# Optimization experiments

Hardware: AMD Instinct MI355X
Metric: run time of the kernel (lower is better)

The kernel has to match this reference:

```python
import jax, jax.numpy as jnp
from jax import lax
import numpy as np

WIN = 8          # window side -> N = 64 tokens per window
DIM = 256
HEADS = 8
B_ = 4096        # batch * num_windows
DN = ('NCHW', 'OIHW', 'NCHW')


def _rel_pos_index(win):
    ch = np.arange(win)
    coords = np.stack(np.meshgrid(ch, ch, indexing='ij'))
    flat = coords.reshape(2, -1)
    rel = flat[:, :, None] - flat[:, None, :]                      # [2,N,N]
    rel = rel.transpose(1, 2, 0).astype(np.int32)                  # [N,N,2]
    rel[..., 0] += win - 1
    rel[..., 1] += win - 1
    rel[..., 0] *= 2 * win - 1
    return rel.sum(-1)                                             # [N,N] in [0, (2w-1)^2)


def _sepconv(x, dw_w, dw_b, pw_w, pw_b):
    # x: [B,C,H,W]; depthwise 3x3 (groups=C) + bias + ReLU, then pointwise 1x1 + bias
    C = x.shape[1]
    y = lax.conv_general_dilated(x, dw_w, (1, 1), [(1, 1), (1, 1)],
                                 dimension_numbers=DN, feature_group_count=C)
    y = jax.nn.relu(y + dw_b[None, :, None, None])
    y = lax.conv_general_dilated(y, pw_w, (1, 1), [(0, 0), (0, 0)],
                                 dimension_numbers=DN)
    return y + pw_b[None, :, None, None]


def setup_inputs() -> dict:
    key = jax.random.key(0)
    ks = jax.random.split(key, 16)
    C = DIM
    d = {}
    d['x'] = jax.random.normal(ks[0], (B_, WIN * WIN, C), dtype=jnp.float32)
    for i, p in enumerate(['q', 'k', 'v']):
        d[f'{p}_dw_w'] = jax.random.normal(ks[1 + 4 * i], (C, 1, 3, 3), jnp.float32) * 0.05
        d[f'{p}_dw_b'] = jax.random.normal(ks[2 + 4 * i], (C,), jnp.float32) * 0.02
        d[f'{p}_pw_w'] = jax.random.normal(ks[3 + 4 * i], (C, C, 1, 1), jnp.float32) * 0.05
        d[f'{p}_pw_b'] = jax.random.normal(ks[4 + 4 * i], (C,), jnp.float32) * 0.02
    d['bias_table'] = jax.random.normal(ks[13], ((2 * WIN - 1) ** 2, HEADS), jnp.float32) * 0.02
    d['proj_w'] = jax.random.normal(ks[14], (C, C), jnp.float32) * 0.02
    d['proj_b'] = jax.random.normal(ks[15], (C,), jnp.float32) * 0.02
    d['rel_index'] = jnp.asarray(_rel_pos_index(WIN))  # [N,N] int32
    return d


def reference(x, q_dw_w, q_dw_b, q_pw_w, q_pw_b,
              k_dw_w, k_dw_b, k_pw_w, k_pw_b,
              v_dw_w, v_dw_b, v_pw_w, v_pw_b,
              bias_table, proj_w, proj_b, rel_index):
    B, N, C = x.shape
    H = HEADS
    dh = C // H
    scale = dh ** (-0.5)
    l = WIN
    xi = x.transpose(0, 2, 1).reshape(B, C, l, l)          # b (l w) c -> b c l w
    q = _sepconv(xi, q_dw_w, q_dw_b, q_pw_w, q_pw_b)
    k = _sepconv(xi, k_dw_w, k_dw_b, k_pw_w, k_pw_b)
    v = _sepconv(xi, v_dw_w, v_dw_b, v_pw_w, v_pw_b)
    # b (h d) l w -> b h (l w) d
    q = q.reshape(B, H, dh, N).transpose(0, 1, 3, 2)
    k = k.reshape(B, H, dh, N).transpose(0, 1, 3, 2)
    v = v.reshape(B, H, dh, N).transpose(0, 1, 3, 2)
    attn = jnp.einsum('bhnd,bhmd->bhnm', q * scale, k)     # [B,H,N,N]
    bias = bias_table[rel_index]                           # [N,N,H] gather
    attn = attn + bias.transpose(2, 0, 1)[None]            # ratio=1, repeat is identity
    attn = jax.nn.softmax(attn, axis=-1)
    out = jnp.einsum('bhnm,bhmd->bhnd', attn, v)           # [B,H,N,dh]
    out = out.transpose(0, 2, 1, 3).reshape(B, N, C)
    return out @ proj_w.T + proj_b
```

## Files before the change

### kernel.cpp

```cpp
#include <hip/hip_runtime.h>

typedef __attribute__((ext_vector_type(8))) short bf16x8;
typedef __attribute__((ext_vector_type(4))) float f32x4;

#define XK_B 0
#define S_B  32768
#define Q_B  49152

__device__ __forceinline__ unsigned short f2b(float f) {
  unsigned int v = __builtin_bit_cast(unsigned int, f);
  v += 0x7FFFu + ((v >> 16) & 1u);
  return (unsigned short)(v >> 16);
}
__device__ __forceinline__ unsigned int pk2(float a, float b) {
  return (unsigned int)f2b(a) | ((unsigned int)f2b(b) << 16);
}
__device__ __forceinline__ bf16x8 pack8(const float4& a, const float4& b) {
  union { unsigned int u[4]; bf16x8 v; } x;
  x.u[0] = pk2(a.x, a.y); x.u[1] = pk2(a.z, a.w);
  x.u[2] = pk2(b.x, b.y); x.u[3] = pk2(b.z, b.w);
  return x.v;
}
__device__ __forceinline__ float lo16(unsigned int u) { return __builtin_bit_cast(float, u << 16); }
__device__ __forceinline__ float hi16(unsigned int u) { return __builtin_bit_cast(float, u & 0xFFFF0000u); }

__global__ void transpose_dw_kernel(const float* __restrict__ w0,
                                    const float* __restrict__ w1,
                                    const float* __restrict__ w2,
                                    float* __restrict__ out) {
  int i = blockIdx.x * 256 + threadIdx.x;
  if (i >= 6912) return;
  int p = i / 2304, r = i % 2304, tap = r >> 8, c = r & 255;
  const float* w = (p == 0) ? w0 : ((p == 1) ? w1 : w2);
  out[i] = w[c * 9 + tap];
}

template<int USE_WS>
__global__ __launch_bounds__(512, 2) void winattn_kernel(
    const float* __restrict__ xg,
    const float* __restrict__ dww0, const float* __restrict__ dwb0,
    const float* __restrict__ pww0, const float* __restrict__ pwb0,
    const float* __restrict__ dww1, const float* __restrict__ dwb1,
    const float* __restrict__ pww1, const float* __restrict__ pwb1,
    const float* __restrict__ dww2, const float* __restrict__ dwb2,
    const float* __restrict__ pww2, const float* __restrict__ pwb2,
    const float* __restrict__ bt,
    const float* __restrict__ pjw, const float* __restrict__ pjb,
    const int* __restrict__ rel,
    const float* __restrict__ wsT,
    float* __restrict__ outg)
{
  __shared__ __align__(16) unsigned char smem[81920];

  const int tid  = threadIdx.x;
  const int lane = tid & 63;
  const int wv   = tid >> 6;
  const int lc   = lane & 15;
  const int lq2  = lane >> 4;
  const int b    = blockIdx.x;
  const float* xb = xg + (size_t)b * 16384;

  const f32x4 zero4 = {0.f, 0.f, 0.f, 0.f};

#pragma unroll
  for (int it = 0; it < 4; ++it) {
    const int g   = tid + it * 512;
    const int n   = g >> 5;
    const int c16 = g & 31;
    const float4 wa = *(const float4*)(xb + n * 256 + c16 * 8);
    const float4 wb = *(const float4*)(xb + n * 256 + c16 * 8 + 4);
    *(bf16x8*)(smem + XK_B + n * 512 + ((c16 ^ (n & 7))) * 16) = pack8(wa, wb);
  }
  __syncthreads();

  auto dwconv = [&](int s, const float* __restrict__ dwb,
                    const float* __restrict__ dwwT, const float* __restrict__ dwwR) {
    const int c4    = tid & 31;
    const int strip = tid >> 5;
    const int l   = strip >> 1;
    const int w0c = (strip & 1) * 4;
    const int cb  = s * 128 + c4 * 4;
    const int c16 = s * 16 + (c4 >> 1);
    const int hb8 = (c4 & 1) * 8;
    float o[4][4];
    {
      const f32x4 bv = *(const f32x4*)(dwb + cb);
#pragma unroll
      for (int t = 0; t < 4; ++t)
#pragma unroll
        for (int j = 0; j < 4; ++j) o[t][j] = bv[j];
    }
#pragma unroll
    for (int dl = 0; dl < 3; ++dl) {
      const int row = l + dl - 1;
      const bool rok = (row >= 0) && (row < 8);
      float wt[3][4];
#pragma unroll
      for (int dc = 0; dc < 3; ++dc) {
        if (USE_WS) {
          const f32x4 wv0 = *(const f32x4*)(dwwT + (dl * 3 + dc) * 256 + cb);
#pragma unroll
          for (int j = 0; j < 4; ++j) wt[dc][j] = wv0[j];
        } else {
#pragma unroll
          for (int j = 0; j < 4; ++j) wt[dc][j] = dwwR[(cb + j) * 9 + dl * 3 + dc];
        }
      }
#pragma unroll
      for (int jc = 0; jc < 6; ++jc) {
        const int col = w0c + jc - 1;
        float xc[4];
        if (rok && col >= 0 && col < 8) {
          const int t = row * 8 + col;
          const uint2 u = *(const uint2*)(smem + XK_B + t * 512 + ((c16 ^ (t & 7))) * 16 + hb8);
          xc[0] = lo16(u.x); xc[1] = hi16(u.x);
          xc[2] = lo16(u.y); xc[3] = hi16(u.y);
        } else {
#pragma unroll
          for (int j = 0; j < 4; ++j) xc[j] = 0.f;
        }
#pragma unroll
        for (int dc = 0; dc < 3; ++dc) {
          const int ot = jc - dc;
          if (ot >= 0 && ot < 4) {
#pragma unroll
            for (int j = 0; j < 4; ++j) o[ot][j] = fmaf(wt[dc][j], xc[j], o[ot][j]);
          }
        }
      }
    }
#pragma unroll
    for (int t = 0; t < 4; ++t) {
      const int n = l * 8 + w0c + t;
      uint2 u;
      u.x = pk2(fmaxf(o[t][0], 0.f), fmaxf(o[t][1], 0.f));
      u.y = pk2(fmaxf(o[t][2], 0.f), fmaxf(o[t][3], 0.f));
      *(uint2*)(smem + S_B + n * 256 + (((c4 >> 1) ^ (n & 15)) & 15) * 16 + hb8) = u;
    }
  };

  bf16x8 vfrag[2][2];
  {
    f32x4 av[4][2];
#pragma unroll
    for (int i = 0; i < 4; ++i)
#pragma unroll
      for (int t = 0; t < 2; ++t) av[i][t] = zero4;

#pragma unroll 1
    for (int s = 0; s < 2; ++s) {
      dwconv(s, dwb2, USE_WS ? (wsT + 2 * 2304) : nullptr, dww2);
      __syncthreads();
      const float* W = pww2;
#pragma unroll
      for (int kk = 0; kk < 4; ++kk) {
        bf16x8 afr[4];
#pragma unroll
        for (int i = 0; i < 4; ++i) {
          const int m = 16 * i + lc;
          afr[i] = *(const bf16x8*)(smem + S_B + m * 256 + (((4 * kk + lq2) ^ (m & 15)) & 15) * 16);
        }
        bf16x8 bb[2];
#pragma unroll
        for (int t = 0; t < 2; ++t) {
          const int co = 16 * (2 * wv + t) + lc;
          const int ci0 = s * 128 + 32 * kk + 8 * lq2;
          const float4 wa = *(const float4*)(W + co * 256 + ci0);
          const float4 wb = *(const float4*)(W + co * 256 + ci0 + 4);
          bb[t] = pack8(wa, wb);
        }
#pragma unroll
        for (int i = 0; i < 4; ++i)
#pragma unroll
          for (int t = 0; t < 2; ++t)
            av[i][t] = __builtin_amdgcn_mfma_f32_16x16x32_bf16(afr[i], bb[t], av[i][t], 0, 0, 0);
      }
      __syncthreads();
    }
#pragma unroll
    for (int t = 0; t < 2; ++t) {
      const float pb = pwb2[16 * (2 * wv + t) + lc];
#pragma unroll
      for (int i = 0; i < 4; ++i) {
        const int m0 = 16 * i + 4 * lq2;
        uint2 u;
        u.x = pk2(av[i][t][0] + pb, av[i][t][1] + pb);
        u.y = pk2(av[i][t][2] + pb, av[i][t][3] + pb);
        *(uint2*)(smem + S_B + wv * 2048 + lc * 128 +
                  (((m0 >> 3) ^ (lc & 7)) & 7) * 16 + (lq2 & 1) * 8) = u;
      }
#pragma unroll
      for (int kk = 0; kk < 2; ++kk)
        vfrag[t][kk] = *(const bf16x8*)(smem + S_B + wv * 2048 + lc * 128 +
                                        (((4 * kk + lq2) ^ (lc & 7)) & 7) * 16);
    }
  }
  __syncthreads();

#pragma unroll 1
  for (int qk = 0; qk < 2; ++qk) {
    const int dstB = qk ? XK_B : Q_B;
    const float* W   = qk ? pww1 : pww0;
    const float* pwb = qk ? pwb1 : pwb0;
    const float* dwb = qk ? dwb1 : dwb0;
    const float* dwT = USE_WS ? (wsT + qk * 2304) : nullptr;
    const float* dwR = qk ? dww1 : dww0;
    f32x4 acc[2][4];
#pragma unroll
    for (int cot = 0; cot < 2; ++cot)
#pragma unroll
      for (int nt = 0; nt < 4; ++nt) acc[cot][nt] = zero4;

#pragma unroll 1
    for (int s = 0; s < 2; ++s) {
      dwconv(s, dwb, dwT, dwR);
      __syncthreads();
#pragma unroll
      for (int kk = 0; kk < 4; ++kk) {
        bf16x8 afrW[2];
#pragma unroll
        for (int cot = 0; cot < 2; ++cot) {
          const int co = 32 * wv + 16 * cot + lc;
          const int ci0 = s * 128 + 32 * kk + 8 * lq2;
          const float4 wa = *(const float4*)(W + co * 256 + ci0);
          const float4 wb = *(const float4*)(W + co * 256 + ci0 + 4);
          afrW[cot] = pack8(wa, wb);
        }
        bf16x8 bfr[4];
#pragma unroll
        for (int nt = 0; nt < 4; ++nt) {
          const int n = 16 * nt + lc;
          bfr[nt] = *(const bf16x8*)(smem + S_B + n * 256 + (((4 * kk + lq2) ^ (n & 15)) & 15) * 16);
        }
#pragma unroll
        for (int cot = 0; cot < 2; ++cot)
#pragma unroll
          for (int nt = 0; nt < 4; ++nt)
            acc[cot][nt] = __builtin_amdgcn_mfma_f32_16x16x32_bf16(afrW[cot], bfr[nt], acc[cot][nt], 0, 0, 0);
      }
      __syncthreads();
    }
#pragma unroll
    for (int cot = 0; cot < 2; ++cot) {
      const int c0 = 32 * wv + 16 * cot + 4 * lq2;
      const f32x4 pb = *(const f32x4*)(pwb + c0);
#pragma unroll
      for (int nt = 0; nt < 4; ++nt) {
        const int n = 16 * nt + lc;
        uint2 u;
        u.x = pk2(acc[cot][nt][0] + pb[0], acc[cot][nt][1] + pb[1]);
        u.y = pk2(acc[cot][nt][2] + pb[2], acc[cot][nt][3] + pb[3]);
        *(uint2*)(smem + dstB + n * 512 + (((c0 >> 3) ^ (n & 31)) & 31) * 16 + (lq2 & 1) * 8) = u;
      }
    }
  }

  {
    const int h = wv;
    bf16x8 kfrag[4];
#pragma unroll
    for (int mt = 0; mt < 4; ++mt) {
      const int m = 16 * mt + lc;
      kfrag[mt] = *(const bf16x8*)(smem + XK_B + m * 512 + (((4 * h + lq2) ^ (m & 31)) & 31) * 16);
    }
    const float scale = 0.17677669529663687f;
#pragma unroll
    for (int qt = 0; qt < 4; ++qt) {
      const int n = 16 * qt + lc;
      const bf16x8 qfrag = *(const bf16x8*)(smem + Q_B + n * 512 + (((4 * h + lq2) ^ (n & 31)) & 31) * 16);
      f32x4 sc[4];
#pragma unroll
      for (int mt = 0; mt < 4; ++mt)
        sc[mt] = __builtin_amdgcn_mfma_f32_16x16x32_bf16(kfrag[mt], qfrag, zero4, 0, 0, 0);
      const int* relrow = rel + n * 64;
      float sv[4][4];
#pragma unroll
      for (int mt = 0; mt < 4; ++mt)
#pragma unroll
        for (int r = 0; r < 4; ++r) {
          const int m = 16 * mt + 4 * lq2 + r;
          sv[mt][r] = sc[mt][r] * scale + bt[relrow[m] * 8 + h];
        }
      float mx = sv[0][0];
#pragma unroll
      for (int mt = 0; mt < 4; ++mt)
#pragma unroll
        for (int r = 0; r < 4; ++r) mx = fmaxf(mx, sv[mt][r]);
      mx = fmaxf(mx, __shfl_xor(mx, 16));
      mx = fmaxf(mx, __shfl_xor(mx, 32));
      float sum = 0.f;
#pragma unroll
      for (int mt = 0; mt < 4; ++mt)
#pragma unroll
        for (int r = 0; r < 4; ++r) {
          sv[mt][r] = __expf(sv[mt][r] - mx);
          sum += sv[mt][r];
        }
      sum += __shfl_xor(sum, 16);
      sum += __shfl_xor(sum, 32);
      const float rinv = __builtin_amdgcn_rcpf(sum);
#pragma unroll
      for (int mt = 0; mt < 4; ++mt) {
        const int m0 = 16 * mt + 4 * lq2;
        uint2 u;
        u.x = pk2(sv[mt][0], sv[mt][1]);
        u.y = pk2(sv[mt][2], sv[mt][3]);
        *(uint2*)(smem + S_B + wv * 2048 + lc * 128 +
                  (((m0 >> 3) ^ (lc & 7)) & 7) * 16 + (lq2 & 1) * 8) = u;
      }
      f32x4 o[2] = {zero4, zero4};
#pragma unroll
      for (int kk = 0; kk < 2; ++kk) {
        const bf16x8 pf = *(const bf16x8*)(smem + S_B + wv * 2048 + lc * 128 +
                                           (((4 * kk + lq2) ^ (lc & 7)) & 7) * 16);
#pragma unroll
        for (int ct = 0; ct < 2; ++ct)
          o[ct] = __builtin_amdgcn_mfma_f32_16x16x32_bf16(vfrag[ct][kk], pf, o[ct], 0, 0, 0);
      }
#pragma unroll
      for (int ct = 0; ct < 2; ++ct) {
        const int c0 = 32 * h + 16 * ct + 4 * lq2;
        uint2 u;
        u.x = pk2(o[ct][0] * rinv, o[ct][1] * rinv);
        u.y = pk2(o[ct][2] * rinv, o[ct][3] * rinv);
        *(uint2*)(smem + XK_B + n * 512 + (((c0 >> 3) ^ (n & 31)) & 31) * 16 + (lq2 & 1) * 8) = u;
      }
    }
  }
  __syncthreads();

  {
    f32x4 pacc[4][2];
#pragma unroll
    for (int i = 0; i < 4; ++i)
#pragma unroll
      for (int t = 0; t < 2; ++t) pacc[i][t] = zero4;
#pragma unroll
    for (int kk = 0; kk < 8; ++kk) {
      bf16x8 afr[4];
#pragma unroll
      for (int i = 0; i < 4; ++i) {
        const int n = 16 * i + lc;
        afr[i] = *(const bf16x8*)(smem + XK_B + n * 512 + (((4 * kk + lq2) ^ (n & 31)) & 31) * 16);
      }
      bf16x8 bb[2];
#pragma unroll
      for (int t = 0; t < 2; ++t) {
        const int co = 16 * (2 * wv + t) + lc;
        const float4 wa = *(const float4*)(pjw + co * 256 + 32 * kk + 8 * lq2);
        const float4 wb = *(const float4*)(pjw + co * 256 + 32 * kk + 8 * lq2 + 4);
        bb[t] = pack8(wa, wb);
      }
#pragma unroll
      for (int i = 0; i < 4; ++i)
#pragma unroll
        for (int t = 0; t < 2; ++t)
          pacc[i][t] = __builtin_amdgcn_mfma_f32_16x16x32_bf16(afr[i], bb[t], pacc[i][t], 0, 0, 0);
    }
    float* og = outg + (size_t)b * 16384;
#pragma unroll
    for (int t = 0; t < 2; ++t) {
      const int co = 16 * (2 * wv + t) + lc;
      const float pbv = pjb[co];
#pragma unroll
      for (int i = 0; i < 4; ++i)
#pragma unroll
        for (int r = 0; r < 4; ++r)
          og[(16 * i + 4 * lq2 + r) * 256 + co] = pacc[i][t][r] + pbv;
    }
  }
}

extern "C" void kernel_launch(void* const* d_in, const int* in_sizes, int n_in,
                              void* d_out, int out_size, void* d_ws, size_t ws_size,
                              hipStream_t stream) {
  (void)in_sizes; (void)n_in; (void)out_size;
  const float* x    = (const float*)d_in[0];
  const float* qdww = (const float*)d_in[1];
  const float* qdwb = (const float*)d_in[2];
  const float* qpww = (const float*)d_in[3];
  const float* qpwb = (const float*)d_in[4];
  const float* kdww = (const float*)d_in[5];
  const float* kdwb = (const float*)d_in[6];
  const float* kpww = (const float*)d_in[7];
  const float* kpwb = (const float*)d_in[8];
  const float* vdww = (const float*)d_in[9];
  const float* vdwb = (const float*)d_in[10];
  const float* vpww = (const float*)d_in[11];
  const float* vpwb = (const float*)d_in[12];
  const float* bt   = (const float*)d_in[13];
  const float* pjw  = (const float*)d_in[14];
  const float* pjb  = (const float*)d_in[15];
  const int* rel    = (const int*)d_in[16];
  float* out        = (float*)d_out;

  const bool use_ws = (ws_size >= 6912 * sizeof(float)) && (d_ws != nullptr);
  float* wsT = (float*)d_ws;

  if (use_ws) {
    hipLaunchKernelGGL(transpose_dw_kernel, dim3(27), dim3(256), 0, stream,
                       qdww, kdww, vdww, wsT);
    hipLaunchKernelGGL((winattn_kernel<1>), dim3(4096), dim3(512), 0, stream,
                       x, qdww, qdwb, qpww, qpwb, kdww, kdwb, kpww, kpwb,
                       vdww, vdwb, vpww, vpwb, bt, pjw, pjb, rel, wsT, out);
  } else {
    hipLaunchKernelGGL((winattn_kernel<0>), dim3(4096), dim3(512), 0, stream,
                       x, qdww, qdwb, qpww, qpwb, kdww, kdwb, kpww, kpwb,
                       vdww, vdwb, vpww, vpwb, bt, pjw, pjb, rel, (const float*)nullptr, out);
  }
}
```

Measured before the change: 954.8 us.

## Split fused window attention into QKV and attention+projection kernels via workspace

Splits the single fused kernel into two. The first computes the Q/K/V separable convolutions and writes bf16 fragments to a large global workspace (about 400MB). The second reads those fragments, runs attention with the relative-position bias and softmax, then applies the output projection. This is meant to cut shared memory per block (49KB instead of 80KB) so more blocks fit per CU, at the cost of extra global memory traffic. The split path runs only when the harness workspace is large enough; otherwise the fused kernel is used.

```diff
diff --git a/kernel.cpp b/kernel.cpp
--- a/kernel.cpp
+++ b/kernel.cpp
@@ -6,6 +6,10 @@
 #define XK_B 0
 #define S_B  32768
 #define Q_B  49152
+#define K1_S 32768
+#define K2_P 32768
+
+#define QWS_SHORTS 67108864ull
 
 __device__ __forceinline__ unsigned short f2b(float f) {
   unsigned int v = __builtin_bit_cast(unsigned int, f);
@@ -35,6 +39,363 @@
   out[i] = w[c * 9 + tap];
 }
 
+__global__ __launch_bounds__(512, 2) void qkv_kernel(
+    const float* __restrict__ xg,
+    const float* __restrict__ dwb0, const float* __restrict__ pww0, const float* __restrict__ pwb0,
+    const float* __restrict__ dwb1, const float* __restrict__ pww1, const float* __restrict__ pwb1,
+    const float* __restrict__ dwb2, const float* __restrict__ pww2, const float* __restrict__ pwb2,
+    const float* __restrict__ dwT,
+    unsigned short* __restrict__ qkv)
+{
+  __shared__ __align__(16) unsigned char smem[49152];
+  const int tid  = threadIdx.x;
+  const int lane = tid & 63;
+  const int wv   = tid >> 6;
+  const int lc   = lane & 15;
+  const int lq2  = lane >> 4;
+  const int b    = blockIdx.x;
+  const float* xb = xg + (size_t)b * 16384;
+  const f32x4 zero4 = {0.f, 0.f, 0.f, 0.f};
+
+#pragma unroll
+  for (int it = 0; it < 4; ++it) {
+    const int g   = tid + it * 512;
+    const int n   = g >> 5;
+    const int c16 = g & 31;
+    const float4 wa = *(const float4*)(xb + n * 256 + c16 * 8);
+    const float4 wb = *(const float4*)(xb + n * 256 + c16 * 8 + 4);
+    *(bf16x8*)(smem + XK_B + n * 512 + ((c16 ^ (n & 7))) * 16) = pack8(wa, wb);
+  }
+  __syncthreads();
+
+  auto dwconv = [&](int s, const float* __restrict__ dwb, const float* __restrict__ dT) {
+    const int c4    = tid & 31;
+    const int strip = tid >> 5;
+    const int l   = strip >> 1;
+    const int w0c = (strip & 1) * 4;
+    const int cb  = s * 128 + c4 * 4;
+    const int c16 = s * 16 + (c4 >> 1);
+    const int hb8 = (c4 & 1) * 8;
+    float o[4][4];
+    {
+      const f32x4 bv = *(const f32x4*)(dwb + cb);
+#pragma unroll
+      for (int t = 0; t < 4; ++t)
+#pragma unroll
+        for (int j = 0; j < 4; ++j) o[t][j] = bv[j];
+    }
+#pragma unroll
+    for (int dl = 0; dl < 3; ++dl) {
+      const int row = l + dl - 1;
+      const bool rok = (row >= 0) && (row < 8);
+      float wt[3][4];
+#pragma unroll
+      for (int dc = 0; dc < 3; ++dc) {
+        const f32x4 wv0 = *(const f32x4*)(dT + (dl * 3 + dc) * 256 + cb);
+#pragma unroll
+        for (int j = 0; j < 4; ++j) wt[dc][j] = wv0[j];
+      }
+#pragma unroll
+      for (int jc = 0; jc < 6; ++jc) {
+        const int col = w0c + jc - 1;
+        float xc[4];
+        if (rok && col >= 0 && col < 8) {
+          const int t = row * 8 + col;
+          const uint2 u = *(const uint2*)(smem + XK_B + t * 512 + ((c16 ^ (t & 7))) * 16 + hb8);
+          xc[0] = lo16(u.x); xc[1] = hi16(u.x);
+          xc[2] = lo16(u.y); xc[3] = hi16(u.y);
+        } else {
+#pragma unroll
+          for (int j = 0; j < 4; ++j) xc[j] = 0.f;
+        }
+#pragma unroll
+        for (int dc = 0; dc < 3; ++dc) {
+          const int ot = jc - dc;
+          if (ot >= 0 && ot < 4) {
+#pragma unroll
+            for (int j = 0; j < 4; ++j) o[ot][j] = fmaf(wt[dc][j], xc[j], o[ot][j]);
+          }
+        }
+      }
+    }
+#pragma unroll
+    for (int t = 0; t < 4; ++t) {
+      const int n = l * 8 + w0c + t;
+      uint2 u;
+      u.x = pk2(fmaxf(o[t][0], 0.f), fmaxf(o[t][1], 0.f));
+      u.y = pk2(fmaxf(o[t][2], 0.f), fmaxf(o[t][3], 0.f));
+      *(uint2*)(smem + K1_S + n * 256 + (((c4 >> 1) ^ (n & 15)) & 15) * 16 + hb8) = u;
+    }
+  };
+
+#pragma unroll 1
+  for (int qk = 0; qk < 2; ++qk) {
+    const float* W   = qk ? pww1 : pww0;
+    const float* pwb = qk ? pwb1 : pwb0;
+    const float* dwb = qk ? dwb1 : dwb0;
+    const float* dT  = dwT + qk * 2304;
+    f32x4 acc[2][4];
+#pragma unroll
+    for (int cot = 0; cot < 2; ++cot)
+#pragma unroll
+      for (int nt = 0; nt < 4; ++nt) acc[cot][nt] = zero4;
+
+#pragma unroll 1
+    for (int s = 0; s < 2; ++s) {
+      dwconv(s, dwb, dT);
+      __syncthreads();
+#pragma unroll
+      for (int kk = 0; kk < 4; ++kk) {
+        bf16x8 afrW[2];
+#pragma unroll
+        for (int cot = 0; cot < 2; ++cot) {
+          const int co = 32 * wv + 16 * cot + lc;
+          const int ci0 = s * 128 + 32 * kk + 8 * lq2;
+          const float4 wa = *(const float4*)(W + co * 256 + ci0);
+          const float4 wb = *(const float4*)(W + co * 256 + ci0 + 4);
+          afrW[cot] = pack8(wa, wb);
+        }
+        bf16x8 bfr[4];
+#pragma unroll
+        for (int nt = 0; nt < 4; ++nt) {
+          const int n = 16 * nt + lc;
+          bfr[nt] = *(const bf16x8*)(smem + K1_S + n * 256 + (((4 * kk + lq2) ^ (n & 15)) & 15) * 16);
+        }
+#pragma unroll
+        for (int cot = 0; cot < 2; ++cot)
+#pragma unroll
+          for (int nt = 0; nt < 4; ++nt)
+            acc[cot][nt] = __builtin_amdgcn_mfma_f32_16x16x32_bf16(afrW[cot], bfr[nt], acc[cot][nt], 0, 0, 0);
+      }
+      __syncthreads();
+    }
+    unsigned short* dst = qkv + (qk ? QWS_SHORTS : 0) + ((size_t)(b * 8 + wv) * 4) * 512;
+    unsigned char* Sb = smem + K1_S + wv * 2048;
+#pragma unroll
+    for (int rr = 0; rr < 2; ++rr) {
+#pragma unroll
+      for (int cot = 0; cot < 2; ++cot) {
+        const int c0 = 32 * wv + 16 * cot + 4 * lq2;
+        const f32x4 pb = *(const f32x4*)(pwb + c0);
+        const int o8 = 2 * cot + (lq2 >> 1);
+#pragma unroll
+        for (int nt2 = 0; nt2 < 2; ++nt2) {
+          const int nt = 2 * rr + nt2;
+          const int nn = 16 * nt2 + lc;
+          uint2 u;
+          u.x = pk2(acc[cot][nt][0] + pb[0], acc[cot][nt][1] + pb[1]);
+          u.y = pk2(acc[cot][nt][2] + pb[2], acc[cot][nt][3] + pb[3]);
+          *(uint2*)(Sb + nn * 64 + ((o8 ^ (nn & 3)) * 16) + (lq2 & 1) * 8) = u;
+        }
+      }
+#pragma unroll
+      for (int mtl = 0; mtl < 2; ++mtl) {
+        const int nn = 16 * mtl + lc;
+        const bf16x8 fr = *(const bf16x8*)(Sb + nn * 64 + ((lq2 ^ (nn & 3)) * 16));
+        *(bf16x8*)(dst + (2 * rr + mtl) * 512 + lane * 8) = fr;
+      }
+    }
+    __syncthreads();
+  }
+
+  {
+    f32x4 av[4][2];
+#pragma unroll
+    for (int i = 0; i < 4; ++i)
+#pragma unroll
+      for (int t = 0; t < 2; ++t) av[i][t] = zero4;
+
+#pragma unroll 1
+    for (int s = 0; s < 2; ++s) {
+      dwconv(s, dwb2, dwT + 2 * 2304);
+      __syncthreads();
+#pragma unroll
+      for (int kk = 0; kk < 4; ++kk) {
+        bf16x8 afr[4];
+#pragma unroll
+        for (int i = 0; i < 4; ++i) {
+          const int m = 16 * i + lc;
+          afr[i] = *(const bf16x8*)(smem + K1_S + m * 256 + (((4 * kk + lq2) ^ (m & 15)) & 15) * 16);
+        }
+        bf16x8 bb[2];
+#pragma unroll
+        for (int t = 0; t < 2; ++t) {
+          const int co = 16 * (2 * wv + t) + lc;
+          const int ci0 = s * 128 + 32 * kk + 8 * lq2;
+          const float4 wa = *(const float4*)(pww2 + co * 256 + ci0);
+          const float4 wb = *(const float4*)(pww2 + co * 256 + ci0 + 4);
+          bb[t] = pack8(wa, wb);
+        }
+#pragma unroll
+        for (int i = 0; i < 4; ++i)
+#pragma unroll
+          for (int t = 0; t < 2; ++t)
+            av[i][t] = __builtin_amdgcn_mfma_f32_16x16x32_bf16(afr[i], bb[t], av[i][t], 0, 0, 0);
+      }
+      __syncthreads();
+    }
+    unsigned short* dst = qkv + 2 * QWS_SHORTS + ((size_t)(b * 8 + wv) * 4) * 512;
+#pragma unroll
+    for (int t = 0; t < 2; ++t) {
+      const float pb = pwb2[16 * (2 * wv + t) + lc];
+#pragma unroll
+      for (int i = 0; i < 4; ++i) {
+        const int m0 = 16 * i + 4 * lq2;
+        uint2 u;
+        u.x = pk2(av[i][t][0] + pb, av[i][t][1] + pb);
+        u.y = pk2(av[i][t][2] + pb, av[i][t][3] + pb);
+        *(uint2*)(smem + K1_S + wv * 2048 + lc * 128 +
+                  (((m0 >> 3) ^ (lc & 7)) & 7) * 16 + (lq2 & 1) * 8) = u;
+      }
+#pragma unroll
+      for (int kk = 0; kk < 2; ++kk) {
+        const bf16x8 vf = *(const bf16x8*)(smem + K1_S + wv * 2048 + lc * 128 +
+                                           (((4 * kk + lq2) ^ (lc & 7)) & 7) * 16);
+        *(bf16x8*)(dst + (t * 2 + kk) * 512 + lane * 8) = vf;
+      }
+    }
+  }
+}
+
+__global__ __launch_bounds__(512, 2) void attnproj_kernel(
+    const unsigned short* __restrict__ qkv,
+    const float* __restrict__ bt,
+    const float* __restrict__ pjw, const float* __restrict__ pjb,
+    const int* __restrict__ rel,
+    float* __restrict__ outg)
+{
+  __shared__ __align__(16) unsigned char smem[49152];
+  const int tid  = threadIdx.x;
+  const int lane = tid & 63;
+  const int wv   = tid >> 6;
+  const int lc   = lane & 15;
+  const int lq2  = lane >> 4;
+  const int b    = blockIdx.x;
+  const f32x4 zero4 = {0.f, 0.f, 0.f, 0.f};
+
+  const unsigned short* qw = qkv + ((size_t)(b * 8 + wv) * 4) * 512;
+  const unsigned short* kw = qw + QWS_SHORTS;
+  const unsigned short* vw = qw + 2 * QWS_SHORTS;
+
+  bf16x8 kfrag[4];
+#pragma unroll
+  for (int mt = 0; mt < 4; ++mt)
+    kfrag[mt] = *(const bf16x8*)(kw + mt * 512 + lane * 8);
+  bf16x8 vfrag[2][2];
+#pragma unroll
+  for (int t = 0; t < 2; ++t)
+#pragma unroll
+    for (int kk = 0; kk < 2; ++kk)
+      vfrag[t][kk] = *(const bf16x8*)(vw + (t * 2 + kk) * 512 + lane * 8);
+
+  const float scale = 0.17677669529663687f;
+  const int h = wv;
+#pragma unroll
+  for (int qt = 0; qt < 4; ++qt) {
+    const int n = 16 * qt + lc;
+    const bf16x8 qfrag = *(const bf16x8*)(qw + qt * 512 + lane * 8);
+    f32x4 sc[4];
+#pragma unroll
+    for (int mt = 0; mt < 4; ++mt)
+      sc[mt] = __builtin_amdgcn_mfma_f32_16x16x32_bf16(kfrag[mt], qfrag, zero4, 0, 0, 0);
+    const int* relrow = rel + n * 64;
+    float sv[4][4];
+#pragma unroll
+    for (int mt = 0; mt < 4; ++mt)
+#pragma unroll
+      for (int r = 0; r < 4; ++r) {
+        const int m = 16 * mt + 4 * lq2 + r;
+        sv[mt][r] = sc[mt][r] * scale + bt[relrow[m] * 8 + h];
+      }
+    float mx = sv[0][0];
+#pragma unroll
+    for (int mt = 0; mt < 4; ++mt)
+#pragma unroll
+      for (int r = 0; r < 4; ++r) mx = fmaxf(mx, sv[mt][r]);
+    mx = fmaxf(mx, __shfl_xor(mx, 16));
+    mx = fmaxf(mx, __shfl_xor(mx, 32));
+    float sum = 0.f;
+#pragma unroll
+    for (int mt = 0; mt < 4; ++mt)
+#pragma unroll
+      for (int r = 0; r < 4; ++r) {
+        sv[mt][r] = __expf(sv[mt][r] - mx);
+        sum += sv[mt][r];
+      }
+    sum += __shfl_xor(sum, 16);
+    sum += __shfl_xor(sum, 32);
+    const float rinv = __builtin_amdgcn_rcpf(sum);
+#pragma unroll
+    for (int mt = 0; mt < 4; ++mt) {
+      const int m0 = 16 * mt + 4 * lq2;
+      uint2 u;
+      u.x = pk2(sv[mt][0], sv[mt][1]);
+      u.y = pk2(sv[mt][2], sv[mt][3]);
+      *(uint2*)(smem + K2_P + wv * 2048 + lc * 128 +
+                (((m0 >> 3) ^ (lc & 7)) & 7) * 16 + (lq2 & 1) * 8) = u;
+    }
+    f32x4 o[2] = {zero4, zero4};
+#pragma unroll
+    for (int kk = 0; kk < 2; ++kk) {
+      const bf16x8 pf = *(const bf16x8*)(smem + K2_P + wv * 2048 + lc * 128 +
+                                         (((4 * kk + lq2) ^ (lc & 7)) & 7) * 16);
+#pragma unroll
+      for (int ct = 0; ct < 2; ++ct)
+        o[ct] = __builtin_amdgcn_mfma_f32_16x16x32_bf16(vfrag[ct][kk], pf, o[ct], 0, 0, 0);
+    }
+#pragma unroll
+    for (int ct = 0; ct < 2; ++ct) {
+      const int c0 = 32 * h + 16 * ct + 4 * lq2;
+      uint2 u;
+      u.x = pk2(o[ct][0] * rinv, o[ct][1] * rinv);
+      u.y = pk2(o[ct][2] * rinv, o[ct][3] * rinv);
+      *(uint2*)(smem + n * 512 + (((c0 >> 3) ^ (n & 31)) & 31) * 16 + (lq2 & 1) * 8) = u;
+    }
+  }
+  __syncthreads();
+
+  {
+    f32x4 pacc[4][2];
+#pragma unroll
+    for (int i = 0; i < 4; ++i)
+#pragma unroll
+      for (int t = 0; t < 2; ++t) pacc[i][t] = zero4;
+#pragma unroll
+    for (int kk = 0; kk < 8; ++kk) {
+      bf16x8 afr[4];
+#pragma unroll
+      for (int i = 0; i < 4; ++i) {
+        const int n = 16 * i + lc;
+        afr[i] = *(const bf16x8*)(smem + n * 512 + (((4 * kk + lq2) ^ (n & 31)) & 31) * 16);
+      }
+      bf16x8 bb[2];
+#pragma unroll
+      for (int t = 0; t < 2; ++t) {
+        const int co = 16 * (2 * wv + t) + lc;
+        const float4 wa = *(const float4*)(pjw + co * 256 + 32 * kk + 8 * lq2);
+        const float4 wb = *(const float4*)(pjw + co * 256 + 32 * kk + 8 * lq2 + 4);
+        bb[t] = pack8(wa, wb);
+      }
+#pragma unroll
+      for (int i = 0; i < 4; ++i)
+#pragma unroll
+        for (int t = 0; t < 2; ++t)
+          pacc[i][t] = __builtin_amdgcn_mfma_f32_16x16x32_bf16(afr[i], bb[t], pacc[i][t], 0, 0, 0);
+    }
+    float* og = outg + (size_t)b * 16384;
+#pragma unroll
+    for (int t = 0; t < 2; ++t) {
+      const int co = 16 * (2 * wv + t) + lc;
+      const float pbv = pjb[co];
+#pragma unroll
+      for (int i = 0; i < 4; ++i)
+#pragma unroll
+        for (int r = 0; r < 4; ++r)
+          og[(16 * i + 4 * lq2 + r) * 256 + co] = pacc[i][t][r] + pbv;
+    }
+  }
+}
+
 template<int USE_WS>
 __global__ __launch_bounds__(512, 2) void winattn_kernel(
     const float* __restrict__ xg,
@@ -51,7 +412,6 @@
     float* __restrict__ outg)
 {
   __shared__ __align__(16) unsigned char smem[81920];
-
   const int tid  = threadIdx.x;
   const int lane = tid & 63;
   const int wv   = tid >> 6;
@@ -59,7 +419,6 @@
   const int lq2  = lane >> 4;
   const int b    = blockIdx.x;
   const float* xb = xg + (size_t)b * 16384;
-
   const f32x4 zero4 = {0.f, 0.f, 0.f, 0.f};
 
 #pragma unroll
@@ -146,12 +505,10 @@
     for (int i = 0; i < 4; ++i)
 #pragma unroll
       for (int t = 0; t < 2; ++t) av[i][t] = zero4;
-
 #pragma unroll 1
     for (int s = 0; s < 2; ++s) {
       dwconv(s, dwb2, USE_WS ? (wsT + 2 * 2304) : nullptr, dww2);
       __syncthreads();
-      const float* W = pww2;
 #pragma unroll
       for (int kk = 0; kk < 4; ++kk) {
         bf16x8 afr[4];
@@ -165,8 +522,8 @@
         for (int t = 0; t < 2; ++t) {
           const int co = 16 * (2 * wv + t) + lc;
           const int ci0 = s * 128 + 32 * kk + 8 * lq2;
-          const float4 wa = *(const float4*)(W + co * 256 + ci0);
-          const float4 wb = *(const float4*)(W + co * 256 + ci0 + 4);
+          const float4 wa = *(const float4*)(pww2 + co * 256 + ci0);
+          const float4 wb = *(const float4*)(pww2 + co * 256 + ci0 + 4);
           bb[t] = pack8(wa, wb);
         }
 #pragma unroll
@@ -210,7 +567,6 @@
     for (int cot = 0; cot < 2; ++cot)
 #pragma unroll
       for (int nt = 0; nt < 4; ++nt) acc[cot][nt] = zero4;
-
 #pragma unroll 1
     for (int s = 0; s < 2; ++s) {
       dwconv(s, dwb, dwT, dwR);
@@ -394,10 +750,18 @@
   const int* rel    = (const int*)d_in[16];
   float* out        = (float*)d_out;
 
-  const bool use_ws = (ws_size >= 6912 * sizeof(float)) && (d_ws != nullptr);
-  float* wsT = (float*)d_ws;
-
-  if (use_ws) {
+  const size_t SPLIT_WS = 32768ull + 3ull * QWS_SHORTS * 2ull;
+  if (ws_size >= SPLIT_WS && d_ws != nullptr) {
+    float* wsT = (float*)d_ws;
+    unsigned short* qkv = (unsigned short*)((char*)d_ws + 32768);
+    hipLaunchKernelGGL(transpose_dw_kernel, dim3(27), dim3(256), 0, stream,
+                       qdww, kdww, vdww, wsT);
+    hipLaunchKernelGGL(qkv_kernel, dim3(4096), dim3(512), 0, stream,
+                       x, qdwb, qpww, qpwb, kdwb, kpww, kpwb, vdwb, vpww, vpwb, wsT, qkv);
+    hipLaunchKernelGGL(attnproj_kernel, dim3(4096), dim3(512), 0, stream,
+                       qkv, bt, pjw, pjb, rel, out);
+  } else if (ws_size >= 27648 && d_ws != nullptr) {
+    float* wsT = (float*)d_ws;
     hipLaunchKernelGGL(transpose_dw_kernel, dim3(27), dim3(256), 0, stream,
                        qdww, kdww, vdww, wsT);
     hipLaunchKernelGGL((winattn_kernel<1>), dim3(4096), dim3(512), 0, stream,
```

Measured after the change: 986.2 us. 1.03x slower.
